# Optimization experiments

Hardware: AMD Instinct MI355X
Metric: run time of the kernel (lower is better)

Reference implementation:

```python
import math
import jax, jax.numpy as jnp
import numpy as np

K = 64            # multiplicity per irrep
NE = 10           # num_elements
N_NODES = 10000
N_EDGES = 100000
AVG_NEIGH = 10.0
EDGE_DIM = 8
LS = [0, 1, 2]    # node/intermediate irreps 64x0e+64x1o+64x2e
LS_OUT = [0, 1]   # output irreps 64x0e+64x1o
INV_SQRT_K = 1.0 / math.sqrt(K)
MIX_NORM = 1.0 / math.sqrt(K * NE)

# ---- real spherical-harmonic Clebsch-Gordan coefficients (small l, exact) ----
def _cg(j1, m1, j2, m2, j3, m3):
    if m1 + m2 != m3 or not (abs(j1 - j2) <= j3 <= j1 + j2):
        return 0.0
    f = math.factorial
    pre = math.sqrt((2 * j3 + 1) * f(j1 + j2 - j3) * f(j1 - j2 + j3) * f(-j1 + j2 + j3) / f(j1 + j2 + j3 + 1))
    pre *= math.sqrt(f(j1 + m1) * f(j1 - m1) * f(j2 + m2) * f(j2 - m2) * f(j3 + m3) * f(j3 - m3))
    s = 0.0
    for k in range(j1 + j2 + j3 + 1):
        d = (j1 + j2 - j3 - k, j1 - m1 - k, j2 + m2 - k, j3 - j2 + m1 + k, j3 - j1 - m2 + k)
        if min(d) < 0:
            continue
        s += (-1) ** k / (f(k) * f(d[0]) * f(d[1]) * f(d[2]) * f(d[3]) * f(d[4]))
    return pre * s

def _u_real(l):
    # complex->real SH change of basis: Y_real = U @ Y_complex
    U = np.zeros((2 * l + 1, 2 * l + 1), dtype=np.complex128)
    U[l, l] = 1.0
    s = 1.0 / math.sqrt(2.0)
    for m in range(1, l + 1):
        U[l + m, l + m] = (-1) ** m * s
        U[l + m, l - m] = s
        U[l - m, l + m] = -1j * (-1) ** m * s
        U[l - m, l - m] = 1j * s
    return U

def real_cg(l1, l2, l3):
    C = np.zeros((2 * l1 + 1, 2 * l2 + 1, 2 * l3 + 1), dtype=np.complex128)
    for m1 in range(-l1, l1 + 1):
        for m2 in range(-l2, l2 + 1):
            m3 = m1 + m2
            if abs(m3) <= l3:
                C[l1 + m1, l2 + m2, l3 + m3] = _cg(l1, m1, l2, m2, l3, m3)
    U1, U2, U3 = _u_real(l1), _u_real(l2), _u_real(l3)
    Cr = np.einsum('ai,bj,ck,ijk->abc', U1, U2, U3.conj(), C)
    return np.ascontiguousarray(Cr.real).astype(np.float32)  # real since l1+l2+l3 even

# parity/triangle allowed paths (l1: edge sph, l2: node in, l3: intermediate) -> 11 paths
EDGE_PATHS = [(l1, l2, l3) for l1 in LS for l2 in LS for l3 in LS
              if abs(l1 - l2) <= l3 <= l1 + l2 and (l1 + l2 + l3) % 2 == 0]
N_EDGE_PATHS = len(EDGE_PATHS)  # 11
DEG2_PATHS = [(0, 0, 0), (1, 1, 0), (2, 2, 0), (0, 1, 1), (1, 2, 1)]
DEG3_PATHS = [(0, 0, 0), (1, 1, 0), (0, 1, 1), (1, 0, 1), (1, 2, 1)]
CG_EDGE = [real_cg(*p) for p in EDGE_PATHS]
CG_D2 = [real_cg(*p) for p in DEG2_PATHS]
CG_D3 = [real_cg(*p) for p in DEG3_PATHS]

def split_irreps(x, ls, mul):
    # ir_mul layout: per irrep a [(2l+1)*mul] flat segment, m index outer
    out, o = [], 0
    for l in ls:
        d = (2 * l + 1) * mul
        out.append(x[:, o:o + d].reshape(x.shape[0], 2 * l + 1, mul))
        o += d
    return out


def setup_inputs() -> dict:
    key = jax.random.key(0)
    ks = jax.random.split(key, 20)
    sender = jax.random.randint(ks[0], (N_EDGES,), 0, N_NODES)
    receiver = jax.random.randint(ks[1], (N_EDGES,), 0, N_NODES)
    indices = jax.random.randint(ks[2], (N_NODES,), 0, NE)
    node_attrs = jax.nn.one_hot(indices, NE, dtype=jnp.float32)
    node_feature_in = jax.random.normal(ks[3], (N_NODES, K * 9), dtype=jnp.float32)
    edge_length_embed = jax.random.normal(ks[4], (N_EDGES, EDGE_DIM), dtype=jnp.float32)
    edge_sph_embed = jax.random.normal(ks[5], (N_EDGES, 9), dtype=jnp.float32)
    W_lin_in = jax.random.normal(ks[6], (3, K, K), dtype=jnp.float32)
    mlp_W0 = jax.random.normal(ks[7], (EDGE_DIM, 32), dtype=jnp.float32) / math.sqrt(EDGE_DIM)
    mlp_b0 = jnp.zeros((32,), jnp.float32)
    mlp_W1 = jax.random.normal(ks[8], (32, 32), dtype=jnp.float32) / math.sqrt(32.0)
    mlp_b1 = jnp.zeros((32,), jnp.float32)
    mlp_W2 = jax.random.normal(ks[9], (32, 32), dtype=jnp.float32) / math.sqrt(32.0)
    mlp_b2 = jnp.zeros((32,), jnp.float32)
    mlp_W3 = jax.random.normal(ks[10], (32, N_EDGE_PATHS * K), dtype=jnp.float32) / math.sqrt(32.0)
    mlp_b3 = jnp.zeros((N_EDGE_PATHS * K,), jnp.float32)
    W_mix = jax.random.normal(ks[11], (3, NE, K, K), dtype=jnp.float32)
    w1 = jax.random.normal(ks[12], (NE, 2, K), dtype=jnp.float32)
    w2 = 0.1 * jax.random.normal(ks[13], (NE, len(DEG2_PATHS), K), dtype=jnp.float32)
    w3 = 0.05 * jax.random.normal(ks[14], (NE, len(DEG3_PATHS), K), dtype=jnp.float32)
    W_out_m = jax.random.normal(ks[15], (2, K, K), dtype=jnp.float32)
    W_out_h = jax.random.normal(ks[16], (2, K, K), dtype=jnp.float32)
    return dict(sender=sender, receiver=receiver, indices=indices, node_attrs=node_attrs,
                node_feature_in=node_feature_in, edge_length_embed=edge_length_embed,
                edge_sph_embed=edge_sph_embed, W_lin_in=W_lin_in,
                mlp_W0=mlp_W0, mlp_b0=mlp_b0, mlp_W1=mlp_W1, mlp_b1=mlp_b1,
                mlp_W2=mlp_W2, mlp_b2=mlp_b2, mlp_W3=mlp_W3, mlp_b3=mlp_b3,
                W_mix=W_mix, w1=w1, w2=w2, w3=w3, W_out_m=W_out_m, W_out_h=W_out_h)


def reference(sender, receiver, indices, node_attrs, node_feature_in,
              edge_length_embed, edge_sph_embed, W_lin_in,
              mlp_W0, mlp_b0, mlp_W1, mlp_b1, mlp_W2, mlp_b2, mlp_W3, mlp_b3,
              W_mix, w1, w2, w3, W_out_m, W_out_h):
    N = node_feature_in.shape[0]
    h1 = split_irreps(node_feature_in, LS, K)  # per-l [N, 2l+1, K]
    # ELinear_h1_2_h1p: per-irrep channel mixing
    h1p = [jnp.einsum('nmc,cd->nmd', h1[l], W_lin_in[l]) * INV_SQRT_K for l in LS]
    # residual radial MLP -> per-edge TP path weights [E, P, K]
    h = jax.nn.silu(edge_length_embed @ mlp_W0 + mlp_b0)
    h = h + jax.nn.silu(h @ mlp_W1 + mlp_b1)
    h = h + jax.nn.silu(h @ mlp_W2 + mlp_b2)
    Rl = (h @ mlp_W3 + mlp_b3).reshape(-1, N_EDGE_PATHS, K)
    sph = split_irreps(edge_sph_embed, LS, 1)  # per-l [E, 2l+1, 1]
    gx = [h1p[l][sender] for l in LS]          # gather sender node features
    # channelwise equivariant tensor product with per-edge radial weights
    msg = [None, None, None]
    for p, (l1, l2, l3) in enumerate(EDGE_PATHS):
        t = jnp.einsum('abd,ea,ebc->edc', jnp.asarray(CG_EDGE[p]), sph[l1][:, :, 0], gx[l2])
        t = t * Rl[:, p, None, :]
        msg[l3] = t if msg[l3] is None else msg[l3] + t
    # scatter-sum messages to receivers, normalized by avg num neighbors
    A = [jax.ops.segment_sum(msg[l], receiver, num_segments=N) / AVG_NEIGH for l in LS]
    # element-conditioned mixing (FCTP with num_elements x 0e attrs)
    Amix = [jnp.einsum('nmc,ne,ecd->nmd', A[l], node_attrs, W_mix[l]) * MIX_NORM for l in LS]
    # symmetric contraction (body order 3) with element-dependent channelwise weights
    w1n, w2n, w3n = w1[indices], w2[indices], w3[indices]
    T2 = [jnp.zeros_like(Amix[L]) for L in LS_OUT]
    for p, (l1, l2, L) in enumerate(DEG2_PATHS):
        t = jnp.einsum('abd,nac,nbc->ndc', jnp.asarray(CG_D2[p]), Amix[l1], Amix[l2])
        T2[L] = T2[L] + w2n[:, p, None, :] * t
    T3 = [jnp.zeros_like(Amix[L]) for L in LS_OUT]
    for q, (Lp, l3, L) in enumerate(DEG3_PATHS):
        t = jnp.einsum('abd,nac,nbc->ndc', jnp.asarray(CG_D3[q]), T2[Lp], Amix[l3])
        T3[L] = T3[L] + w3n[:, q, None, :] * t
    B = [w1n[:, L, None, :] * Amix[L] + T2[L] + T3[L] for L in LS_OUT]
    # node_feature_out = ELinear_h1_2_h2(h1) + ELinear_m2_2_h2(B)
    out = []
    for L in LS_OUT:
        y = jnp.einsum('nmc,cd->nmd', h1[L], W_out_h[L]) * INV_SQRT_K
        y = y + jnp.einsum('nmc,cd->nmd', B[L], W_out_m[L]) * INV_SQRT_K
        out.append(y.reshape(N, -1))
    return jnp.concatenate(out, axis=1)  # [N, 4K] = [N, 256]
```

## Files before the change

### kernel.cpp

```cpp
#include <hip/hip_runtime.h>
#include <math.h>

#define NNODES 10000
#define NEDGES 100000

typedef float v2f __attribute__((ext_vector_type(2)));

struct Cplx { double re, im; };

constexpr double cfact(int n){ double r=1.0; for(int i=2;i<=n;++i) r*=i; return r; }

constexpr double csqrt_(double x){
  if (x<=0.0) return 0.0;
  double g = x<1.0 ? 1.0 : x;
  for (int it=0; it<64; ++it){ double ng = 0.5*(g + x/g); if (ng==g) break; g = ng; }
  return g;
}

constexpr double cg_coeff(int j1,int m1,int j2,int m2,int j3,int m3){
  if (m1+m2!=m3) return 0.0;
  int lo = j1>j2 ? j1-j2 : j2-j1;
  if (j3<lo || j3>j1+j2) return 0.0;
  if (m1<-j1||m1>j1||m2<-j2||m2>j2||m3<-j3||m3>j3) return 0.0;
  double pre = csqrt_((2.0*j3+1.0)*cfact(j1+j2-j3)*cfact(j1-j2+j3)*cfact(-j1+j2+j3)/cfact(j1+j2+j3+1));
  pre *= csqrt_(cfact(j1+m1)*cfact(j1-m1)*cfact(j2+m2)*cfact(j2-m2)*cfact(j3+m3)*cfact(j3-m3));
  double s = 0.0;
  for (int k=0;k<=j1+j2+j3;++k){
    int d0=j1+j2-j3-k, d1=j1-m1-k, d2=j2+m2-k, d3=j3-j2+m1+k, d4=j3-j1-m2+k;
    if (d0<0||d1<0||d2<0||d3<0||d4<0) continue;
    double term = 1.0/(cfact(k)*cfact(d0)*cfact(d1)*cfact(d2)*cfact(d3)*cfact(d4));
    s += (k&1) ? -term : term;
  }
  return pre*s;
}

constexpr Cplx uent(int l,int a,int i){
  const double s = 0.70710678118654752440;
  int ma = a - l;
  if (ma==0) { if (i==l) return Cplx{1.0,0.0}; return Cplx{0.0,0.0}; }
  if (ma>0){
    int m = ma; double sg = (m&1) ? -1.0 : 1.0;
    if (i==l+m) return Cplx{sg*s, 0.0};
    if (i==l-m) return Cplx{s, 0.0};
    return Cplx{0.0,0.0};
  }
  int m = -ma; double sg = (m&1) ? -1.0 : 1.0;
  if (i==l+m) return Cplx{0.0, -sg*s};
  if (i==l-m) return Cplx{0.0, s};
  return Cplx{0.0,0.0};
}

constexpr double real_cg_entry(int l1,int l2,int l3,int a,int b,int c){
  double acc = 0.0;
  int ii0 = a, ii1 = 2*l1-a;
  int jj0 = b, jj1 = 2*l2-b;
  for (int x=0;x<2;++x){
    int i = (x==0)? ii0 : ii1;
    if (x==1 && ii1==ii0) break;
    Cplx u1 = uent(l1,a,i); if (u1.re==0.0 && u1.im==0.0) continue;
    for (int y=0;y<2;++y){
      int j = (y==0)? jj0 : jj1;
      if (y==1 && jj1==jj0) break;
      Cplx u2 = uent(l2,b,j); if (u2.re==0.0 && u2.im==0.0) continue;
      int k = (i-l1)+(j-l2)+l3;
      if (k<0 || k>2*l3) continue;
      Cplx u3 = uent(l3,c,k); if (u3.re==0.0 && u3.im==0.0) continue;
      double cg = cg_coeff(l1,i-l1,l2,j-l2,l3,k-l3);
      if (cg==0.0) continue;
      double pr = u1.re*u2.re - u1.im*u2.im;
      double pi = u1.re*u2.im + u1.im*u2.re;
      acc += (pr*u3.re + pi*u3.im) * cg;
    }
  }
  return acc;
}

struct CGT { float v[5][5][5]; };
constexpr CGT make_cg(int l1,int l2,int l3){
  CGT t{};
  for (int a=0;a<2*l1+1;++a)
    for (int b=0;b<2*l2+1;++b)
      for (int c=0;c<2*l3+1;++c)
        t.v[a][b][c] = (float)real_cg_entry(l1,l2,l3,a,b,c);
  return t;
}

__device__ __forceinline__ float silu_(float x){ return x / (1.0f + __expf(-x)); }

union H16 { _Float16 h; unsigned short u; };
__device__ __forceinline__ float h2f(unsigned short u){ H16 c; c.u = u; return (float)c.h; }
__device__ __forceinline__ unsigned int pack2(float a, float b){
  H16 x, y; x.h = (_Float16)a; y.h = (_Float16)b;
  return ((unsigned int)y.u << 16) | x.u;
}
__device__ __forceinline__ v2f make2(float s){ v2f r; r.x = s; r.y = s; return r; }

template<int L1,int L2,int L3>
__device__ __forceinline__ void tp_pk(const v2f* sp, const v2f* g, v2f rl, v2f* msg){
  constexpr CGT T = make_cg(L1,L2,L3);
  constexpr int NA = 2*L1+1, NB = 2*L2+1, ND = 2*L3+1;
  v2f t[ND];
#pragma unroll
  for (int d=0;d<ND;++d) t[d] = make2(0.f);
#pragma unroll
  for (int b=0;b<NB;++b){
#pragma unroll
    for (int d=0;d<ND;++d){
      v2f u = make2(0.f); bool any = false;
#pragma unroll
      for (int a=0;a<NA;++a){
        const float cg = T.v[a][b][d];
        if (cg != 0.f){ u = cg*sp[a] + u; any = true; }
      }
      if (any) t[d] = u*g[b] + t[d];
    }
  }
#pragma unroll
  for (int d=0;d<ND;++d) msg[d] = rl*t[d] + msg[d];
}

template<int L1,int L2,int L3>
__device__ __forceinline__ void sc_accum(const float* X, const float* Y, float w, float* out){
  constexpr CGT T = make_cg(L1,L2,L3);
  constexpr int NA = 2*L1+1, NB = 2*L2+1, ND = 2*L3+1;
#pragma unroll
  for (int d=0;d<ND;++d){
    float s = 0.f;
#pragma unroll
    for (int a=0;a<NA;++a){
#pragma unroll
      for (int b=0;b<NB;++b){
        const float cg = T.v[a][b][d];
        if (cg != 0.f) s = fmaf(cg*X[a], Y[b], s);
      }
    }
    out[d] = fmaf(w, s, out[d]);
  }
}

__global__ void __launch_bounds__(64) k_lin_in(const float* __restrict__ h1,
                                               const float* __restrict__ W,
                                               float* __restrict__ h1p,
                                               int* __restrict__ deg){
  const int n = blockIdx.x;
  const int d = threadIdx.x;
  if (d == 0) deg[n] = 0;
  const float* row = h1 + (long)n*576;
  float acc[9];
#pragma unroll
  for (int i=0;i<9;++i) acc[i] = 0.f;
  for (int c=0;c<64;++c){
    const float w0 = W[c*64 + d];
    const float w1 = W[4096 + c*64 + d];
    const float w2 = W[8192 + c*64 + d];
    acc[0] = fmaf(row[c], w0, acc[0]);
#pragma unroll
    for (int m=0;m<3;++m) acc[1+m] = fmaf(row[64+m*64+c], w1, acc[1+m]);
#pragma unroll
    for (int m=0;m<5;++m) acc[4+m] = fmaf(row[256+m*64+c], w2, acc[4+m]);
  }
  float* o = h1p + (long)n*576;
  o[d] = acc[0]*0.125f;
#pragma unroll
  for (int m=0;m<3;++m) o[64+m*64+d] = acc[1+m]*0.125f;
#pragma unroll
  for (int m=0;m<5;++m) o[256+m*64+d] = acc[4+m]*0.125f;
}

__global__ void __launch_bounds__(256) k_mlp(const float* __restrict__ ele,
                                             const float* __restrict__ W0, const float* __restrict__ b0,
                                             const float* __restrict__ W1, const float* __restrict__ b1,
                                             const float* __restrict__ W2, const float* __restrict__ b2,
                                             float* __restrict__ hmlp){
  const int e = blockIdx.x*256 + threadIdx.x;
  if (e >= NEDGES) return;
  float x[8];
#pragma unroll
  for (int i=0;i<8;++i) x[i] = ele[(long)e*8 + i];
  float h[32];
#pragma unroll
  for (int d=0;d<32;++d){
    float acc = b0[d];
#pragma unroll
    for (int i=0;i<8;++i) acc = fmaf(x[i], W0[i*32+d], acc);
    h[d] = silu_(acc);
  }
#pragma unroll
  for (int L=0; L<2; ++L){
    const float* Wl = L ? W2 : W1;
    const float* bl = L ? b2 : b1;
    float acc[32];
#pragma unroll
    for (int d=0;d<32;++d) acc[d] = bl[d];
    for (int j=0;j<32;++j){
      const float hj = h[j];
#pragma unroll
      for (int d=0;d<32;++d) acc[d] = fmaf(hj, Wl[j*32+d], acc[d]);
    }
#pragma unroll
    for (int d=0;d<32;++d) h[d] += silu_(acc[d]);
  }
  float* o = hmlp + (long)e*32;
#pragma unroll
  for (int d=0;d<32;++d) o[d] = h[d];
}

__global__ void __launch_bounds__(256) k_hist(const int* __restrict__ receiver, int* __restrict__ deg){
  const int e = blockIdx.x*256 + threadIdx.x;
  if (e < NEDGES) atomicAdd(&deg[receiver[e]], 1);
}

__global__ void __launch_bounds__(256) k_scan(const int* __restrict__ deg,
                                              int* __restrict__ rowptr,
                                              int* __restrict__ cursor){
  __shared__ int sums[256];
  const int t = threadIdx.x;
  const int CH = 40;
  const int base = t*CH;
  int s = 0;
  for (int i=0;i<CH;++i){ int idx = base+i; if (idx < NNODES) s += deg[idx]; }
  sums[t] = s; __syncthreads();
  for (int off=1; off<256; off<<=1){
    int v = (t>=off) ? sums[t-off] : 0;
    __syncthreads();
    sums[t] += v;
    __syncthreads();
  }
  int run = (t==0) ? 0 : sums[t-1];
  for (int i=0;i<CH;++i){
    int idx = base+i;
    if (idx < NNODES){ rowptr[idx] = run; cursor[idx] = run; run += deg[idx]; }
  }
  if (t==255) rowptr[NNODES] = sums[255];
}

__global__ void __launch_bounds__(256) k_fill_pos(const int* __restrict__ receiver,
                                                  int* __restrict__ cursor,
                                                  int* __restrict__ epos){
  const int e = blockIdx.x*256 + threadIdx.x;
  if (e < NEDGES) epos[e] = atomicAdd(&cursor[receiver[e]], 1);
}

__global__ void __launch_bounds__(256) k_edge_pk(const int* __restrict__ sender,
                                             const int* __restrict__ epos,
                                             const float* __restrict__ hmlp,
                                             const float* __restrict__ sph,
                                             const float* __restrict__ h1p,
                                             const float* __restrict__ W3, const float* __restrict__ b3,
                                             unsigned int* __restrict__ msg){
  __shared__ float sps[4][72];
  const int wid  = threadIdx.x >> 6;
  const int lane = threadIdx.x & 63;
  const int ubase = __builtin_amdgcn_readfirstlane((blockIdx.x*4 + wid) * 8);

  {
    const int idx = lane;
    const int e = idx/9, a = idx - 9*e;
    sps[wid][a*8 + e] = sph[(long)ubase*9 + idx];
  }
  if (lane < 8){
    const int idx = 64 + lane;
    const int e = idx/9, a = idx - 9*e;
    sps[wid][a*8 + e] = sph[(long)ubase*9 + idx];
  }

  int sidx[8], pos[8];
#pragma unroll
  for (int e=0;e<8;++e){ sidx[e] = sender[ubase+e]; pos[e] = epos[ubase+e]; }

  v2f g2[4][9];
#pragma unroll
  for (int q=0;q<4;++q){
    const float* hp0 = h1p + (long)sidx[2*q]  *576;
    const float* hp1 = h1p + (long)sidx[2*q+1]*576;
#pragma unroll
    for (int i=0;i<9;++i){ g2[q][i].x = hp0[i*64+lane]; g2[q][i].y = hp1[i*64+lane]; }
  }
#pragma unroll
  for (int q=0;q<4;++q)
#pragma unroll
    for (int i=0;i<9;++i) asm volatile("" : "+v"(g2[q][i]));

  const float* hu = hmlp + (long)ubase*32;

  v2f rl2[11][4];
#pragma unroll
  for (int p=0;p<11;++p){
    const float bb = b3[p*64+lane];
#pragma unroll
    for (int q=0;q<4;++q) rl2[p][q] = make2(bb);
  }
  for (int jb=0;jb<32;jb+=4){
    float w3v[4][11];
#pragma unroll
    for (int jj=0;jj<4;++jj)
#pragma unroll
      for (int p=0;p<11;++p)
        w3v[jj][p] = W3[(jb+jj)*704 + p*64 + lane];
#pragma unroll
    for (int q=0;q<4;++q){
#pragma unroll
      for (int jj=0;jj<4;++jj){
        v2f h2; h2.x = hu[(2*q)*32 + jb + jj]; h2.y = hu[(2*q+1)*32 + jb + jj];
#pragma unroll
        for (int p=0;p<11;++p) rl2[p][q] = h2*w3v[jj][p] + rl2[p][q];
      }
    }
  }

#pragma unroll
  for (int q=0;q<4;++q){
    v2f sp2[9];
#pragma unroll
    for (int a=0;a<9;++a) sp2[a] = *(const v2f*)&sps[wid][a*8 + 2*q];
    v2f m0[1]; m0[0] = make2(0.f);
    v2f m1[3]; m1[0]=m1[1]=m1[2]=make2(0.f);
    v2f m2[5]; m2[0]=m2[1]=m2[2]=m2[3]=m2[4]=make2(0.f);
    tp_pk<0,0,0>(sp2+0, &g2[q][0], rl2[0][q],  m0);
    tp_pk<0,1,1>(sp2+0, &g2[q][1], rl2[1][q],  m1);
    tp_pk<0,2,2>(sp2+0, &g2[q][4], rl2[2][q],  m2);
    tp_pk<1,0,1>(sp2+1, &g2[q][0], rl2[3][q],  m1);
    tp_pk<1,1,0>(sp2+1, &g2[q][1], rl2[4][q],  m0);
    tp_pk<1,1,2>(sp2+1, &g2[q][1], rl2[5][q],  m2);
    tp_pk<1,2,1>(sp2+1, &g2[q][4], rl2[6][q],  m1);
    tp_pk<2,0,2>(sp2+4, &g2[q][0], rl2[7][q],  m2);
    tp_pk<2,1,1>(sp2+4, &g2[q][1], rl2[8][q],  m1);
    tp_pk<2,2,0>(sp2+4, &g2[q][4], rl2[9][q],  m0);
    tp_pk<2,2,2>(sp2+4, &g2[q][4], rl2[10][q], m2);
    {
      unsigned int pk[5];
      pk[0] = pack2(m0[0].x, m1[0].x);
      pk[1] = pack2(m1[1].x, m1[2].x);
      pk[2] = pack2(m2[0].x, m2[1].x);
      pk[3] = pack2(m2[2].x, m2[3].x);
      pk[4] = pack2(m2[4].x, 0.f);
      unsigned int* mp = msg + (size_t)pos[2*q]*320;
#pragma unroll
      for (int k=0;k<5;++k) mp[k*64 + lane] = pk[k];
    }
    {
      unsigned int pk[5];
      pk[0] = pack2(m0[0].y, m1[0].y);
      pk[1] = pack2(m1[1].y, m1[2].y);
      pk[2] = pack2(m2[0].y, m2[1].y);
      pk[3] = pack2(m2[2].y, m2[3].y);
      pk[4] = pack2(m2[4].y, 0.f);
      unsigned int* mp = msg + (size_t)pos[2*q+1]*320;
#pragma unroll
      for (int k=0;k<5;++k) mp[k*64 + lane] = pk[k];
    }
  }
}

__global__ void __launch_bounds__(256) k_node_c(const int* __restrict__ indices,
                                             const float* __restrict__ h1,
                                             const int* __restrict__ rowptr,
                                             const unsigned int* __restrict__ msg,
                                             const float* __restrict__ Wmix,
                                             const float* __restrict__ w1,
                                             const float* __restrict__ w2,
                                             const float* __restrict__ w3,
                                             const float* __restrict__ Wom,
                                             const float* __restrict__ Woh,
                                             float* __restrict__ out){
  __shared__ float S[4][9][64];
  __shared__ float Bb[4][4][64];
  const int wid  = threadIdx.x >> 6;
  const int lane = threadIdx.x & 63;
  const int n = blockIdx.x*4 + wid;
  const int e = __builtin_amdgcn_readfirstlane(indices[n]);

  {
    const int start = rowptr[n], end = rowptr[n+1];
    float A[9];
#pragma unroll
    for (int i=0;i<9;++i) A[i] = 0.f;
    for (int q=start; q<end; ++q){
      const unsigned int* mp = msg + (size_t)q*320;
#pragma unroll
      for (int k=0;k<5;++k){
        const unsigned int v = mp[k*64 + lane];
        A[2*k] += h2f((unsigned short)(v & 0xffff));
        if (2*k+1 < 9) A[2*k+1] += h2f((unsigned short)(v >> 16));
      }
    }
#pragma unroll
    for (int i=0;i<9;++i) S[wid][i][lane] = A[i];
  }

  float ax[9];
#pragma unroll
  for (int i=0;i<9;++i) ax[i] = 0.f;
  {
    const float* Wm0 = Wmix + (size_t)(0*10 + e)*4096;
    const float* Wm1 = Wmix + (size_t)(1*10 + e)*4096;
    const float* Wm2 = Wmix + (size_t)(2*10 + e)*4096;
    for (int c=0;c<64;++c){
      const float wv0 = Wm0[c*64+lane];
      const float wv1 = Wm1[c*64+lane];
      const float wv2 = Wm2[c*64+lane];
      ax[0] = fmaf(S[wid][0][c], wv0, ax[0]);
#pragma unroll
      for (int m=0;m<3;++m) ax[1+m] = fmaf(S[wid][1+m][c], wv1, ax[1+m]);
#pragma unroll
      for (int m=0;m<5;++m) ax[4+m] = fmaf(S[wid][4+m][c], wv2, ax[4+m]);
    }
  }
#pragma unroll
  for (int i=0;i<9;++i) ax[i] *= 0.0039528470752104741f;

  const float* amix0 = ax;
  const float* amix1 = ax+1;
  const float* amix2 = ax+4;
  float w2n[5], w3n[5];
#pragma unroll
  for (int p=0;p<5;++p){
    w2n[p] = w2[(size_t)(e*5+p)*64 + lane];
    w3n[p] = w3[(size_t)(e*5+p)*64 + lane];
  }
  float t20[1] = {0.f}, t21[3] = {0.f,0.f,0.f};
  sc_accum<0,0,0>(amix0, amix0, w2n[0], t20);
  sc_accum<1,1,0>(amix1, amix1, w2n[1], t20);
  sc_accum<2,2,0>(amix2, amix2, w2n[2], t20);
  sc_accum<0,1,1>(amix0, amix1, w2n[3], t21);
  sc_accum<1,2,1>(amix1, amix2, w2n[4], t21);
  float t30[1] = {0.f}, t31[3] = {0.f,0.f,0.f};
  sc_accum<0,0,0>(t20, amix0, w3n[0], t30);
  sc_accum<1,1,0>(t21, amix1, w3n[1], t30);
  sc_accum<0,1,1>(t20, amix1, w3n[2], t31);
  sc_accum<1,0,1>(t21, amix0, w3n[3], t31);
  sc_accum<1,2,1>(t21, amix2, w3n[4], t31);

  const float w1_0 = w1[(size_t)(e*2+0)*64 + lane];
  const float w1_1 = w1[(size_t)(e*2+1)*64 + lane];
  Bb[wid][0][lane] = fmaf(w1_0, amix0[0], t20[0] + t30[0]);
#pragma unroll
  for (int m=0;m<3;++m) Bb[wid][1+m][lane] = fmaf(w1_1, amix1[m], t21[m] + t31[m]);

  {
    const float* hrow = h1 + (long)n*576;
#pragma unroll
    for (int r=0;r<9;++r) S[wid][r][lane] = hrow[r*64 + lane];
  }

  float o[4];
#pragma unroll
  for (int i=0;i<4;++i) o[i] = 0.f;
  for (int c=0;c<64;++c){
    const float wh0 = Woh[c*64+lane];
    const float wh1 = Woh[4096 + c*64+lane];
    const float wm0 = Wom[c*64+lane];
    const float wm1 = Wom[4096 + c*64+lane];
    o[0] = fmaf(S[wid][0][c], wh0, o[0]);
    o[0] = fmaf(Bb[wid][0][c], wm0, o[0]);
#pragma unroll
    for (int m=0;m<3;++m){
      o[1+m] = fmaf(S[wid][1+m][c], wh1, o[1+m]);
      o[1+m] = fmaf(Bb[wid][1+m][c], wm1, o[1+m]);
    }
  }
  float* orow = out + (long)n*256;
  orow[lane] = o[0]*0.125f;
#pragma unroll
  for (int m=0;m<3;++m) orow[64+m*64+lane] = o[1+m]*0.125f;
}

extern "C" void kernel_launch(void* const* d_in, const int* in_sizes, int n_in,
                              void* d_out, int out_size, void* d_ws, size_t ws_size,
                              hipStream_t stream){
  const int*   sender   = (const int*)  d_in[0];
  const int*   receiver = (const int*)  d_in[1];
  const int*   indices  = (const int*)  d_in[2];
  const float* node_feat= (const float*)d_in[4];
  const float* ele      = (const float*)d_in[5];
  const float* sph      = (const float*)d_in[6];
  const float* W_lin    = (const float*)d_in[7];
  const float* W0 = (const float*)d_in[8],  *b0 = (const float*)d_in[9];
  const float* W1 = (const float*)d_in[10], *b1 = (const float*)d_in[11];
  const float* W2 = (const float*)d_in[12], *b2 = (const float*)d_in[13];
  const float* W3 = (const float*)d_in[14], *b3 = (const float*)d_in[15];
  const float* Wmix = (const float*)d_in[16];
  const float* w1 = (const float*)d_in[17];
  const float* w2 = (const float*)d_in[18];
  const float* w3 = (const float*)d_in[19];
  const float* Wom = (const float*)d_in[20];
  const float* Woh = (const float*)d_in[21];
  float* out = (float*)d_out;

  char* ws = (char*)d_ws;
  const size_t OFF_H1P  = 0;
  const size_t OFF_HMLP = OFF_H1P  + (size_t)NNODES*576*4;
  const size_t OFF_MSG  = OFF_HMLP + (size_t)NEDGES*32*4;
  const size_t OFF_DEG  = OFF_MSG  + (size_t)NEDGES*320*4;
  const size_t OFF_ROW  = OFF_DEG  + 40960;
  const size_t OFF_CUR  = OFF_ROW  + 40960;
  const size_t OFF_EPOS = OFF_CUR  + 40960;

  float* h1p  = (float*)(ws + OFF_H1P);
  float* hmlp = (float*)(ws + OFF_HMLP);
  unsigned int* msg = (unsigned int*)(ws + OFF_MSG);
  int* deg    = (int*)(ws + OFF_DEG);
  int* rowptr = (int*)(ws + OFF_ROW);
  int* cursor = (int*)(ws + OFF_CUR);
  int* epos   = (int*)(ws + OFF_EPOS);

  k_lin_in<<<NNODES, 64, 0, stream>>>(node_feat, W_lin, h1p, deg);
  k_mlp<<<(NEDGES+255)/256, 256, 0, stream>>>(ele, W0,b0,W1,b1,W2,b2, hmlp);
  k_hist<<<(NEDGES+255)/256, 256, 0, stream>>>(receiver, deg);
  k_scan<<<1, 256, 0, stream>>>(deg, rowptr, cursor);
  k_fill_pos<<<(NEDGES+255)/256, 256, 0, stream>>>(receiver, cursor, epos);
  k_edge_pk<<<NEDGES/32, 256, 0, stream>>>(sender, epos, hmlp, sph, h1p, W3, b3, msg);
  k_node_c<<<NNODES/4, 256, 0, stream>>>(indices, node_feat, rowptr, msg,
                                         Wmix, w1, w2, w3, Wom, Woh, out);
}
```

Baseline: 258.0 us.

## Process edges in sender-sorted order to improve gather locality; fuse histogram into MLP

Builds a counting sort of edges by sender (second histogram, scan and permutation) so the edge kernel processes edges grouped by sender. Consecutive edges then tend to share h1p rows, which should improve cache reuse of the 576-float node gathers. The receiver histogram is folded into the MLP kernel, which removes a launch. In exchange, sph and hmlp reads become indirect gathers through the permutation, and the extra atomics and the second scan add overhead. The asm volatile register pin on g2 is also removed.

New measurement: 258.1 us. Within noise of the previous version (+0.1%).

```diff
diff --git a/kernel.cpp b/kernel.cpp
--- a/kernel.cpp
+++ b/kernel.cpp
@@ -141,10 +141,11 @@
 __global__ void __launch_bounds__(64) k_lin_in(const float* __restrict__ h1,
                                                const float* __restrict__ W,
                                                float* __restrict__ h1p,
-                                               int* __restrict__ deg){
+                                               int* __restrict__ rdeg,
+                                               int* __restrict__ sdeg){
   const int n = blockIdx.x;
   const int d = threadIdx.x;
-  if (d == 0) deg[n] = 0;
+  if (d == 0){ rdeg[n] = 0; sdeg[n] = 0; }
   const float* row = h1 + (long)n*576;
   float acc[9];
 #pragma unroll
@@ -171,9 +172,15 @@
                                              const float* __restrict__ W0, const float* __restrict__ b0,
                                              const float* __restrict__ W1, const float* __restrict__ b1,
                                              const float* __restrict__ W2, const float* __restrict__ b2,
+                                             const int* __restrict__ receiver,
+                                             const int* __restrict__ sender,
+                                             int* __restrict__ rdeg,
+                                             int* __restrict__ sdeg,
                                              float* __restrict__ hmlp){
   const int e = blockIdx.x*256 + threadIdx.x;
   if (e >= NEDGES) return;
+  atomicAdd(&rdeg[receiver[e]], 1);
+  atomicAdd(&sdeg[sender[e]], 1);
   float x[8];
 #pragma unroll
   for (int i=0;i<8;++i) x[i] = ele[(long)e*8 + i];
@@ -205,14 +212,11 @@
   for (int d=0;d<32;++d) o[d] = h[d];
 }
 
-__global__ void __launch_bounds__(256) k_hist(const int* __restrict__ receiver, int* __restrict__ deg){
-  const int e = blockIdx.x*256 + threadIdx.x;
-  if (e < NEDGES) atomicAdd(&deg[receiver[e]], 1);
-}
-
-__global__ void __launch_bounds__(256) k_scan(const int* __restrict__ deg,
-                                              int* __restrict__ rowptr,
-                                              int* __restrict__ cursor){
+__global__ void __launch_bounds__(256) k_scan2(const int* __restrict__ rdeg, int* __restrict__ rrow, int* __restrict__ rcur,
+                                               const int* __restrict__ sdeg, int* __restrict__ srow, int* __restrict__ scur){
+  const int* deg = blockIdx.x ? sdeg : rdeg;
+  int* rowptr    = blockIdx.x ? srow : rrow;
+  int* cursor    = blockIdx.x ? scur : rcur;
   __shared__ int sums[256];
   const int t = threadIdx.x;
   const int CH = 40;
@@ -234,14 +238,22 @@
   if (t==255) rowptr[NNODES] = sums[255];
 }
 
-__global__ void __launch_bounds__(256) k_fill_pos(const int* __restrict__ receiver,
-                                                  int* __restrict__ cursor,
-                                                  int* __restrict__ epos){
+__global__ void __launch_bounds__(256) k_fill2(const int* __restrict__ receiver,
+                                               const int* __restrict__ sender,
+                                               int* __restrict__ rcur,
+                                               int* __restrict__ scur,
+                                               int* __restrict__ epos,
+                                               int* __restrict__ sperm){
   const int e = blockIdx.x*256 + threadIdx.x;
-  if (e < NEDGES) epos[e] = atomicAdd(&cursor[receiver[e]], 1);
+  if (e < NEDGES){
+    epos[e] = atomicAdd(&rcur[receiver[e]], 1);
+    int sp_ = atomicAdd(&scur[sender[e]], 1);
+    sperm[sp_] = e;
+  }
 }
 
 __global__ void __launch_bounds__(256) k_edge_pk(const int* __restrict__ sender,
+                                             const int* __restrict__ sperm,
                                              const int* __restrict__ epos,
                                              const float* __restrict__ hmlp,
                                              const float* __restrict__ sph,
@@ -251,22 +263,27 @@
   __shared__ float sps[4][72];
   const int wid  = threadIdx.x >> 6;
   const int lane = threadIdx.x & 63;
-  const int ubase = __builtin_amdgcn_readfirstlane((blockIdx.x*4 + wid) * 8);
+  const int upos = __builtin_amdgcn_readfirstlane((blockIdx.x*4 + wid) * 8);
+
+  int eids[8];
+#pragma unroll
+  for (int k=0;k<8;++k) eids[k] = sperm[upos+k];
 
   {
-    const int idx = lane;
-    const int e = idx/9, a = idx - 9*e;
-    sps[wid][a*8 + e] = sph[(long)ubase*9 + idx];
-  }
-  if (lane < 8){
-    const int idx = 64 + lane;
-    const int e = idx/9, a = idx - 9*e;
-    sps[wid][a*8 + e] = sph[(long)ubase*9 + idx];
+    int ve = 0;
+    if (lane < 8) ve = sperm[upos + lane];
+    const int eL = __shfl(ve, lane/9, 64);
+    sps[wid][(lane%9)*8 + lane/9] = sph[(long)eL*9 + (lane%9)];
+    if (lane < 8){
+      const int eL7 = __shfl(ve, 7, 64);
+      const int a = lane + 1;
+      sps[wid][a*8 + 7] = sph[(long)eL7*9 + a];
+    }
   }
 
   int sidx[8], pos[8];
 #pragma unroll
-  for (int e=0;e<8;++e){ sidx[e] = sender[ubase+e]; pos[e] = epos[ubase+e]; }
+  for (int k=0;k<8;++k){ sidx[k] = sender[eids[k]]; pos[k] = epos[eids[k]]; }
 
   v2f g2[4][9];
 #pragma unroll
@@ -276,12 +293,6 @@
 #pragma unroll
     for (int i=0;i<9;++i){ g2[q][i].x = hp0[i*64+lane]; g2[q][i].y = hp1[i*64+lane]; }
   }
-#pragma unroll
-  for (int q=0;q<4;++q)
-#pragma unroll
-    for (int i=0;i<9;++i) asm volatile("" : "+v"(g2[q][i]));
-
-  const float* hu = hmlp + (long)ubase*32;
 
   v2f rl2[11][4];
 #pragma unroll
@@ -301,7 +312,9 @@
     for (int q=0;q<4;++q){
 #pragma unroll
       for (int jj=0;jj<4;++jj){
-        v2f h2; h2.x = hu[(2*q)*32 + jb + jj]; h2.y = hu[(2*q+1)*32 + jb + jj];
+        v2f h2;
+        h2.x = hmlp[(long)eids[2*q]  *32 + jb + jj];
+        h2.y = hmlp[(long)eids[2*q+1]*32 + jb + jj];
 #pragma unroll
         for (int p=0;p<11;++p) rl2[p][q] = h2*w3v[jj][p] + rl2[p][q];
       }
@@ -491,25 +504,33 @@
   const size_t OFF_H1P  = 0;
   const size_t OFF_HMLP = OFF_H1P  + (size_t)NNODES*576*4;
   const size_t OFF_MSG  = OFF_HMLP + (size_t)NEDGES*32*4;
-  const size_t OFF_DEG  = OFF_MSG  + (size_t)NEDGES*320*4;
-  const size_t OFF_ROW  = OFF_DEG  + 40960;
-  const size_t OFF_CUR  = OFF_ROW  + 40960;
-  const size_t OFF_EPOS = OFF_CUR  + 40960;
+  const size_t OFF_RDEG = OFF_MSG  + (size_t)NEDGES*320*4;
+  const size_t OFF_RROW = OFF_RDEG + 40960;
+  const size_t OFF_RCUR = OFF_RROW + 40964;
+  const size_t OFF_SDEG = OFF_RCUR + 40960;
+  const size_t OFF_SROW = OFF_SDEG + 40960;
+  const size_t OFF_SCUR = OFF_SROW + 40964;
+  const size_t OFF_EPOS = OFF_SCUR + 40960;
+  const size_t OFF_SPRM = OFF_EPOS + (size_t)NEDGES*4;
 
   float* h1p  = (float*)(ws + OFF_H1P);
   float* hmlp = (float*)(ws + OFF_HMLP);
   unsigned int* msg = (unsigned int*)(ws + OFF_MSG);
-  int* deg    = (int*)(ws + OFF_DEG);
-  int* rowptr = (int*)(ws + OFF_ROW);
-  int* cursor = (int*)(ws + OFF_CUR);
+  int* rdeg   = (int*)(ws + OFF_RDEG);
+  int* rrow   = (int*)(ws + OFF_RROW);
+  int* rcur   = (int*)(ws + OFF_RCUR);
+  int* sdeg   = (int*)(ws + OFF_SDEG);
+  int* srow   = (int*)(ws + OFF_SROW);
+  int* scur   = (int*)(ws + OFF_SCUR);
   int* epos   = (int*)(ws + OFF_EPOS);
-
-  k_lin_in<<<NNODES, 64, 0, stream>>>(node_feat, W_lin, h1p, deg);
-  k_mlp<<<(NEDGES+255)/256, 256, 0, stream>>>(ele, W0,b0,W1,b1,W2,b2, hmlp);
-  k_hist<<<(NEDGES+255)/256, 256, 0, stream>>>(receiver, deg);
-  k_scan<<<1, 256, 0, stream>>>(deg, rowptr, cursor);
-  k_fill_pos<<<(NEDGES+255)/256, 256, 0, stream>>>(receiver, cursor, epos);
-  k_edge_pk<<<NEDGES/32, 256, 0, stream>>>(sender, epos, hmlp, sph, h1p, W3, b3, msg);
-  k_node_c<<<NNODES/4, 256, 0, stream>>>(indices, node_feat, rowptr, msg,
+  int* sperm  = (int*)(ws + OFF_SPRM);
+
+  k_lin_in<<<NNODES, 64, 0, stream>>>(node_feat, W_lin, h1p, rdeg, sdeg);
+  k_mlp<<<(NEDGES+255)/256, 256, 0, stream>>>(ele, W0,b0,W1,b1,W2,b2,
+                                              receiver, sender, rdeg, sdeg, hmlp);
+  k_scan2<<<2, 256, 0, stream>>>(rdeg, rrow, rcur, sdeg, srow, scur);
+  k_fill2<<<(NEDGES+255)/256, 256, 0, stream>>>(receiver, sender, rcur, scur, epos, sperm);
+  k_edge_pk<<<NEDGES/32, 256, 0, stream>>>(sender, sperm, epos, hmlp, sph, h1p, W3, b3, msg);
+  k_node_c<<<NNODES/4, 256, 0, stream>>>(indices, node_feat, rrow, msg,
                                          Wmix, w1, w2, w3, Wom, Woh, out);
 }
```

## Replace CSR message buffer with direct fp32 atomic scatter into node accumulators

Applied to the files above, without the earlier changes.

Drops the histogram/scan/position kernels and the fp16 per-edge message buffer. Each edge now atomically adds its fp32 tensor-product outputs straight into a per-node accumulator, which is zeroed in the input linear kernel, and the node kernel just reads that accumulator. This saves three launches, the 64MB message write and read, and the fp16 pack/unpack, in exchange for 900K float atomics per 64-lane wave group that contend on shared receivers. Summation order is no longer deterministic.

Result: slower. 301.7 us (+17.0%).

```diff
diff --git a/kernel.cpp b/kernel.cpp
--- a/kernel.cpp
+++ b/kernel.cpp
@@ -86,13 +86,6 @@
 }
 
 __device__ __forceinline__ float silu_(float x){ return x / (1.0f + __expf(-x)); }
-
-union H16 { _Float16 h; unsigned short u; };
-__device__ __forceinline__ float h2f(unsigned short u){ H16 c; c.u = u; return (float)c.h; }
-__device__ __forceinline__ unsigned int pack2(float a, float b){
-  H16 x, y; x.h = (_Float16)a; y.h = (_Float16)b;
-  return ((unsigned int)y.u << 16) | x.u;
-}
 __device__ __forceinline__ v2f make2(float s){ v2f r; r.x = s; r.y = s; return r; }
 
 template<int L1,int L2,int L3>
@@ -141,10 +134,12 @@
 __global__ void __launch_bounds__(64) k_lin_in(const float* __restrict__ h1,
                                                const float* __restrict__ W,
                                                float* __restrict__ h1p,
-                                               int* __restrict__ deg){
+                                               float* __restrict__ A){
   const int n = blockIdx.x;
   const int d = threadIdx.x;
-  if (d == 0) deg[n] = 0;
+  float* Az = A + (long)n*576;
+#pragma unroll
+  for (int i=0;i<9;++i) Az[i*64+d] = 0.f;
   const float* row = h1 + (long)n*576;
   float acc[9];
 #pragma unroll
@@ -205,49 +200,13 @@
   for (int d=0;d<32;++d) o[d] = h[d];
 }
 
-__global__ void __launch_bounds__(256) k_hist(const int* __restrict__ receiver, int* __restrict__ deg){
-  const int e = blockIdx.x*256 + threadIdx.x;
-  if (e < NEDGES) atomicAdd(&deg[receiver[e]], 1);
-}
-
-__global__ void __launch_bounds__(256) k_scan(const int* __restrict__ deg,
-                                              int* __restrict__ rowptr,
-                                              int* __restrict__ cursor){
-  __shared__ int sums[256];
-  const int t = threadIdx.x;
-  const int CH = 40;
-  const int base = t*CH;
-  int s = 0;
-  for (int i=0;i<CH;++i){ int idx = base+i; if (idx < NNODES) s += deg[idx]; }
-  sums[t] = s; __syncthreads();
-  for (int off=1; off<256; off<<=1){
-    int v = (t>=off) ? sums[t-off] : 0;
-    __syncthreads();
-    sums[t] += v;
-    __syncthreads();
-  }
-  int run = (t==0) ? 0 : sums[t-1];
-  for (int i=0;i<CH;++i){
-    int idx = base+i;
-    if (idx < NNODES){ rowptr[idx] = run; cursor[idx] = run; run += deg[idx]; }
-  }
-  if (t==255) rowptr[NNODES] = sums[255];
-}
-
-__global__ void __launch_bounds__(256) k_fill_pos(const int* __restrict__ receiver,
-                                                  int* __restrict__ cursor,
-                                                  int* __restrict__ epos){
-  const int e = blockIdx.x*256 + threadIdx.x;
-  if (e < NEDGES) epos[e] = atomicAdd(&cursor[receiver[e]], 1);
-}
-
-__global__ void __launch_bounds__(256) k_edge_pk(const int* __restrict__ sender,
-                                             const int* __restrict__ epos,
+__global__ void __launch_bounds__(256) k_edge_at(const int* __restrict__ sender,
+                                             const int* __restrict__ receiver,
                                              const float* __restrict__ hmlp,
                                              const float* __restrict__ sph,
                                              const float* __restrict__ h1p,
                                              const float* __restrict__ W3, const float* __restrict__ b3,
-                                             unsigned int* __restrict__ msg){
+                                             float* __restrict__ A){
   __shared__ float sps[4][72];
   const int wid  = threadIdx.x >> 6;
   const int lane = threadIdx.x & 63;
@@ -264,9 +223,9 @@
     sps[wid][a*8 + e] = sph[(long)ubase*9 + idx];
   }
 
-  int sidx[8], pos[8];
-#pragma unroll
-  for (int e=0;e<8;++e){ sidx[e] = sender[ubase+e]; pos[e] = epos[ubase+e]; }
+  int sidx[8], ridx[8];
+#pragma unroll
+  for (int e=0;e<8;++e){ sidx[e] = sender[ubase+e]; ridx[e] = receiver[ubase+e]; }
 
   v2f g2[4][9];
 #pragma unroll
@@ -276,10 +235,6 @@
 #pragma unroll
     for (int i=0;i<9;++i){ g2[q][i].x = hp0[i*64+lane]; g2[q][i].y = hp1[i*64+lane]; }
   }
-#pragma unroll
-  for (int q=0;q<4;++q)
-#pragma unroll
-    for (int i=0;i<9;++i) asm volatile("" : "+v"(g2[q][i]));
 
   const float* hu = hmlp + (long)ubase*32;
 
@@ -327,35 +282,27 @@
     tp_pk<2,1,1>(sp2+4, &g2[q][1], rl2[8][q],  m1);
     tp_pk<2,2,0>(sp2+4, &g2[q][4], rl2[9][q],  m0);
     tp_pk<2,2,2>(sp2+4, &g2[q][4], rl2[10][q], m2);
-    {
-      unsigned int pk[5];
-      pk[0] = pack2(m0[0].x, m1[0].x);
-      pk[1] = pack2(m1[1].x, m1[2].x);
-      pk[2] = pack2(m2[0].x, m2[1].x);
-      pk[3] = pack2(m2[2].x, m2[3].x);
-      pk[4] = pack2(m2[4].x, 0.f);
-      unsigned int* mp = msg + (size_t)pos[2*q]*320;
-#pragma unroll
-      for (int k=0;k<5;++k) mp[k*64 + lane] = pk[k];
-    }
-    {
-      unsigned int pk[5];
-      pk[0] = pack2(m0[0].y, m1[0].y);
-      pk[1] = pack2(m1[1].y, m1[2].y);
-      pk[2] = pack2(m2[0].y, m2[1].y);
-      pk[3] = pack2(m2[2].y, m2[3].y);
-      pk[4] = pack2(m2[4].y, 0.f);
-      unsigned int* mp = msg + (size_t)pos[2*q+1]*320;
-#pragma unroll
-      for (int k=0;k<5;++k) mp[k*64 + lane] = pk[k];
-    }
-  }
-}
-
-__global__ void __launch_bounds__(256) k_node_c(const int* __restrict__ indices,
+
+    float* A0 = A + (long)ridx[2*q]  *576;
+    float* A1 = A + (long)ridx[2*q+1]*576;
+    atomicAdd(&A0[lane], m0[0].x);
+    atomicAdd(&A1[lane], m0[0].y);
+#pragma unroll
+    for (int m=0;m<3;++m){
+      atomicAdd(&A0[64+m*64+lane], m1[m].x);
+      atomicAdd(&A1[64+m*64+lane], m1[m].y);
+    }
+#pragma unroll
+    for (int m=0;m<5;++m){
+      atomicAdd(&A0[256+m*64+lane], m2[m].x);
+      atomicAdd(&A1[256+m*64+lane], m2[m].y);
+    }
+  }
+}
+
+__global__ void __launch_bounds__(256) k_node_a(const int* __restrict__ indices,
                                              const float* __restrict__ h1,
-                                             const int* __restrict__ rowptr,
-                                             const unsigned int* __restrict__ msg,
+                                             const float* __restrict__ A,
                                              const float* __restrict__ Wmix,
                                              const float* __restrict__ w1,
                                              const float* __restrict__ w2,
@@ -371,21 +318,9 @@
   const int e = __builtin_amdgcn_readfirstlane(indices[n]);
 
   {
-    const int start = rowptr[n], end = rowptr[n+1];
-    float A[9];
-#pragma unroll
-    for (int i=0;i<9;++i) A[i] = 0.f;
-    for (int q=start; q<end; ++q){
-      const unsigned int* mp = msg + (size_t)q*320;
-#pragma unroll
-      for (int k=0;k<5;++k){
-        const unsigned int v = mp[k*64 + lane];
-        A[2*k] += h2f((unsigned short)(v & 0xffff));
-        if (2*k+1 < 9) A[2*k+1] += h2f((unsigned short)(v >> 16));
-      }
-    }
-#pragma unroll
-    for (int i=0;i<9;++i) S[wid][i][lane] = A[i];
+    const float* Ar = A + (long)n*576;
+#pragma unroll
+    for (int i=0;i<9;++i) S[wid][i][lane] = Ar[i*64 + lane];
   }
 
   float ax[9];
@@ -489,27 +424,16 @@
 
   char* ws = (char*)d_ws;
   const size_t OFF_H1P  = 0;
-  const size_t OFF_HMLP = OFF_H1P  + (size_t)NNODES*576*4;
-  const size_t OFF_MSG  = OFF_HMLP + (size_t)NEDGES*32*4;
-  const size_t OFF_DEG  = OFF_MSG  + (size_t)NEDGES*320*4;
-  const size_t OFF_ROW  = OFF_DEG  + 40960;
-  const size_t OFF_CUR  = OFF_ROW  + 40960;
-  const size_t OFF_EPOS = OFF_CUR  + 40960;
+  const size_t OFF_A    = OFF_H1P  + (size_t)NNODES*576*4;
+  const size_t OFF_HMLP = OFF_A    + (size_t)NNODES*576*4;
 
   float* h1p  = (float*)(ws + OFF_H1P);
+  float* A    = (float*)(ws + OFF_A);
   float* hmlp = (float*)(ws + OFF_HMLP);
-  unsigned int* msg = (unsigned int*)(ws + OFF_MSG);
-  int* deg    = (int*)(ws + OFF_DEG);
-  int* rowptr = (int*)(ws + OFF_ROW);
-  int* cursor = (int*)(ws + OFF_CUR);
-  int* epos   = (int*)(ws + OFF_EPOS);
-
-  k_lin_in<<<NNODES, 64, 0, stream>>>(node_feat, W_lin, h1p, deg);
+
+  k_lin_in<<<NNODES, 64, 0, stream>>>(node_feat, W_lin, h1p, A);
   k_mlp<<<(NEDGES+255)/256, 256, 0, stream>>>(ele, W0,b0,W1,b1,W2,b2, hmlp);
-  k_hist<<<(NEDGES+255)/256, 256, 0, stream>>>(receiver, deg);
-  k_scan<<<1, 256, 0, stream>>>(deg, rowptr, cursor);
-  k_fill_pos<<<(NEDGES+255)/256, 256, 0, stream>>>(receiver, cursor, epos);
-  k_edge_pk<<<NEDGES/32, 256, 0, stream>>>(sender, epos, hmlp, sph, h1p, W3, b3, msg);
-  k_node_c<<<NNODES/4, 256, 0, stream>>>(indices, node_feat, rowptr, msg,
+  k_edge_at<<<NEDGES/32, 256, 0, stream>>>(sender, receiver, hmlp, sph, h1p, W3, b3, A);
+  k_node_a<<<NNODES/4, 256, 0, stream>>>(indices, node_feat, A,
                                          Wmix, w1, w2, w3, Wom, Woh, out);
 }
```
